# Performance work log

Hardware: AMD Instinct MI355X
Metric: run time of the kernel (lower is better)

## Reference

```python
import jax, jax.numpy as jnp
import numpy as np

N_NODES = 100000


def gcn_conv(x, W, b, src, dst, n_nodes):
    # PyG GCNConv: x' = D^{-1/2} (A + I) D^{-1/2} (x W) + b, deg counts self-loops
    h = x @ W  # [N, out]
    deg = jax.ops.segment_sum(jnp.ones_like(dst, dtype=h.dtype), dst, num_segments=n_nodes) + 1.0
    dinv = jax.lax.rsqrt(deg)  # [N]
    norm = dinv[src] * dinv[dst]  # per-edge norm [E]
    msg = h[src] * norm[:, None]  # gather + scale, [E, out]
    agg = jax.ops.segment_sum(msg, dst, num_segments=n_nodes)
    agg = agg + h * (dinv * dinv)[:, None]  # self-loop contribution
    return agg + b


def setup_inputs() -> dict:
    key = jax.random.key(0)
    ks = jax.random.split(key, 9)
    N, E, D = N_NODES, 3200000, 165
    x = jax.random.normal(ks[0], (N, D), dtype=jnp.float32)
    edge_index = jax.random.randint(ks[1], (2, E), 0, N, dtype=jnp.int64)
    def glorot(k, fan_in, fan_out):
        lim = np.sqrt(6.0 / (fan_in + fan_out))
        return jax.random.uniform(k, (fan_in, fan_out), jnp.float32, -lim, lim)
    return {
        "x": x,
        "edge_index": edge_index,
        "W1": glorot(ks[2], D, 32), "b1": jnp.zeros((32,), jnp.float32),
        "W2": glorot(ks[3], 32, 16), "b2": jnp.zeros((16,), jnp.float32),
        "W3": glorot(ks[4], 16, 2),  "b3": jnp.zeros((2,), jnp.float32),
    }


def reference(x, edge_index, W1, b1, W2, b2, W3, b3):
    src, dst = edge_index[0], edge_index[1]
    n = x.shape[0]
    h = jax.nn.relu(gcn_conv(x, W1, b1, src, dst, n))
    # dropout p=0.3 is a no-op in eval mode (training=False)
    h = jax.nn.relu(gcn_conv(h, W2, b2, src, dst, n))
    h = gcn_conv(h, W3, b3, src, dst, n)
    return jax.nn.log_softmax(h, axis=1)
```

## Files before the change

### kernel.cpp

```cpp
#include <hip/hip_runtime.h>
#include <math.h>


constexpr int NT = 256;
constexpr int NPB = 256;
constexpr int LOG_NPB = 8;
constexpr int MAXBUK = 512;
constexpr int BSTRIDE = 10240;
constexpr int NREP = 8;
constexpr int SUB = BSTRIDE / NREP;
constexpr int EPB_B = 4096;

typedef __attribute__((ext_vector_type(8))) short bf16x8;
typedef __attribute__((ext_vector_type(4))) float f32x4;

__device__ inline unsigned short f2bf(float f) {
    unsigned u = *(unsigned*)&f;
    u += 0x7fffu + ((u >> 16) & 1u);
    return (unsigned short)(u >> 16);
}
__device__ inline unsigned packbf(float a, float b) {
    return (unsigned)f2bf(a) | ((unsigned)f2bf(b) << 16);
}
__device__ inline void acc8(float* a, uint4 v) {
    const unsigned* u = (const unsigned*)&v;
#pragma unroll
    for (int w = 0; w < 4; w++) {
        unsigned lo = u[w] << 16, hi = u[w] & 0xffff0000u;
        a[2 * w]     += *(float*)&lo;
        a[2 * w + 1] += *(float*)&hi;
    }
}

__global__ __launch_bounds__(NT) void place_kernel(const int* __restrict__ src,
                                                   const int* __restrict__ dst,
                                                   int* __restrict__ cursor8,
                                                   unsigned* __restrict__ ebuf,
                                                   int E, int nbuk) {
    __shared__ int lh[MAXBUK];
    __shared__ int lbase[MAXBUK];
    for (int i = threadIdx.x; i < nbuk; i += NT) lh[i] = 0;
    __syncthreads();
    constexpr int EPT = EPB_B / NT;
    unsigned pk[EPT];
    unsigned bl[EPT];
    int base = blockIdx.x * EPB_B;
    int rep = blockIdx.x & (NREP - 1);
#pragma unroll
    for (int i = 0; i < EPT; i++) {
        int e = base + i * NT + threadIdx.x;
        if (e < E) {
            int s = src[e], d = dst[e];
            int b = d >> LOG_NPB;
            int lp = atomicAdd(&lh[b], 1);
            pk[i] = ((unsigned)(d & (NPB - 1)) << 24) | (unsigned)s;
            bl[i] = ((unsigned)b << 16) | (unsigned)lp;
        } else {
            bl[i] = 0xFFFFFFFFu;
        }
    }
    __syncthreads();
    for (int i = threadIdx.x; i < nbuk; i += NT) {
        int v = lh[i];
        if (v) lbase[i] = atomicAdd(&cursor8[rep * MAXBUK + i], v);
    }
    __syncthreads();
#pragma unroll
    for (int i = 0; i < EPT; i++) {
        if (bl[i] != 0xFFFFFFFFu) {
            int b = (int)(bl[i] >> 16);
            int pos = lbase[b] + (int)(bl[i] & 0xFFFFu);
            if (pos < SUB)
                ebuf[(size_t)b * BSTRIDE + rep * SUB + pos] = pk[i];
        }
    }
}

__global__ __launch_bounds__(NT) void sort_kernel(
    const unsigned* __restrict__ ebuf, const int* __restrict__ cursor8,
    int* __restrict__ esrc, int* __restrict__ rowptr, int* __restrict__ rowcnt,
    float* __restrict__ dinv, int N) {
    __shared__ int cnt[NPB];
    __shared__ int ofs[NPB];
    __shared__ int cur[NPB];
    int tid = threadIdx.x;
    int b = blockIdx.x;
    cnt[tid] = 0;
    __syncthreads();
#pragma unroll
    for (int r = 0; r < NREP; r++) {
        int e0 = b * BSTRIDE + r * SUB;
        int e1 = e0 + min(cursor8[r * MAXBUK + b], SUB);
        for (int i = e0 + tid; i < e1; i += NT)
            atomicAdd(&cnt[ebuf[i] >> 24], 1);
    }
    __syncthreads();
    ofs[tid] = cnt[tid];
    __syncthreads();
    for (int off = 1; off < NPB; off <<= 1) {
        int a = (tid >= off) ? ofs[tid - off] : 0;
        __syncthreads();
        ofs[tid] += a;
        __syncthreads();
    }
    {
        int excl = ofs[tid] - cnt[tid];
        cur[tid] = excl;
        int n = b * NPB + tid;
        if (n < N) {
            rowptr[n] = b * BSTRIDE + excl;
            rowcnt[n] = cnt[tid];
            dinv[n] = rsqrtf((float)cnt[tid] + 1.0f);
        }
    }
    __syncthreads();
#pragma unroll
    for (int r = 0; r < NREP; r++) {
        int e0 = b * BSTRIDE + r * SUB;
        int e1 = e0 + min(cursor8[r * MAXBUK + b], SUB);
        for (int i = e0 + tid; i < e1; i += NT) {
            unsigned p = ebuf[i];
            int l = (int)(p >> 24);
            int pos = atomicAdd(&cur[l], 1);
            esrc[b * BSTRIDE + pos] = (int)(p & 0xFFFFFFu);
        }
    }
}

__global__ __launch_bounds__(NT) void gemm1_mfma(
    const float* __restrict__ in, const float* __restrict__ W,
    const float* __restrict__ dinv, uint4* __restrict__ hs, int Ntot) {
    constexpr int DIN = 165, DOUT = 32;
    __shared__ float tile[4][16][36];
    int lane = threadIdx.x & 63;
    int wv = threadIdx.x >> 6;
    int t = blockIdx.x * 4 + wv;
    int ntiles = (Ntot + 15) >> 4;
    if (t >= ntiles) return;
    int n0 = t << 4;
    int mrow = lane & 15;
    int quad = lane >> 4;
    int arow = n0 + mrow;
    if (arow >= Ntot) arow = Ntot - 1;
    const float* xrow = in + (size_t)arow * DIN;
    f32x4 acc0 = {0.f, 0.f, 0.f, 0.f};
    f32x4 acc1 = {0.f, 0.f, 0.f, 0.f};
#pragma unroll
    for (int c = 0; c < 6; c++) {
        int kb = c * 32 + quad * 8;
        union { bf16x8 v; unsigned short u[8]; } A, B0, B1;
#pragma unroll
        for (int j = 0; j < 8; j++) {
            int k = kb + j;
            float xv = (k < DIN) ? xrow[k] : 0.f;
            float w0 = (k < DIN) ? W[k * DOUT + mrow] : 0.f;
            float w1 = (k < DIN) ? W[k * DOUT + 16 + mrow] : 0.f;
            A.u[j] = f2bf(xv);
            B0.u[j] = f2bf(w0);
            B1.u[j] = f2bf(w1);
        }
        acc0 = __builtin_amdgcn_mfma_f32_16x16x32_bf16(A.v, B0.v, acc0, 0, 0, 0);
        acc1 = __builtin_amdgcn_mfma_f32_16x16x32_bf16(A.v, B1.v, acc1, 0, 0, 0);
    }
#pragma unroll
    for (int r = 0; r < 4; r++) {
        tile[wv][quad * 4 + r][mrow] = acc0[r];
        tile[wv][quad * 4 + r][16 + mrow] = acc1[r];
    }
    int node = lane >> 2;
    int part = lane & 3;
    int n = n0 + node;
    if (n >= Ntot) return;
    float dv = dinv[n];
    float f[8];
#pragma unroll
    for (int i = 0; i < 8; i++) f[i] = tile[wv][node][part * 8 + i];
    unsigned u0 = packbf(dv * f[0], dv * f[1]);
    unsigned u1 = packbf(dv * f[2], dv * f[3]);
    unsigned u2 = packbf(dv * f[4], dv * f[5]);
    unsigned u3 = packbf(dv * f[6], dv * f[7]);
    hs[(size_t)n * 4 + part] = make_uint4(u0, u1, u2, u3);
}

__global__ __launch_bounds__(NT) void g1g2_kernel(
    const uint4* __restrict__ hsb, const int* __restrict__ esrc,
    const int* __restrict__ rowptr, const int* __restrict__ rowcnt,
    const float* __restrict__ dinv, const float* __restrict__ b1,
    const float* __restrict__ W2 , uint4* __restrict__ hs2b,
    int N) {
    __shared__ float sW[32 * 16];
    __shared__ float sb[32];
    for (int i = threadIdx.x; i < 32 * 16; i += NT) sW[i] = W2[i];
    if (threadIdx.x < 32) sb[threadIdx.x] = b1[threadIdx.x];
    __syncthreads();
    int gid = blockIdx.x * NT + threadIdx.x;
    int n = gid >> 2;
    int q = gid & 3;
    int c = q & 1;
    int h = q >> 1;
    if (n >= N) return;
    int start = rowptr[n];
    int cnt = rowcnt[n];
    int half0 = (cnt + 1) >> 1;
    int j    = start + (h ? half0 : 0);
    int jend = start + (h ? cnt : half0);
    float a[16];
    if (h == 0) {
        const uint4* hp = hsb + (size_t)n * 4 + c * 2;
        uint4 v0 = hp[0], v1 = hp[1];
        const unsigned* u0 = (const unsigned*)&v0;
        const unsigned* u1 = (const unsigned*)&v1;
#pragma unroll
        for (int w = 0; w < 4; w++) {
            unsigned lo = u0[w] << 16, hi = u0[w] & 0xffff0000u;
            a[2 * w] = *(float*)&lo; a[2 * w + 1] = *(float*)&hi;
            unsigned lo1 = u1[w] << 16, hi1 = u1[w] & 0xffff0000u;
            a[8 + 2 * w] = *(float*)&lo1; a[8 + 2 * w + 1] = *(float*)&hi1;
        }
    } else {
#pragma unroll
        for (int k = 0; k < 16; k++) a[k] = 0.f;
    }
    for (; j + 3 < jend; j += 4) {
        int s0 = esrc[j], s1 = esrc[j + 1], s2 = esrc[j + 2], s3 = esrc[j + 3];
        uint4 v00 = hsb[(size_t)s0 * 4 + c * 2], v01 = hsb[(size_t)s0 * 4 + c * 2 + 1];
        uint4 v10 = hsb[(size_t)s1 * 4 + c * 2], v11 = hsb[(size_t)s1 * 4 + c * 2 + 1];
        uint4 v20 = hsb[(size_t)s2 * 4 + c * 2], v21 = hsb[(size_t)s2 * 4 + c * 2 + 1];
        uint4 v30 = hsb[(size_t)s3 * 4 + c * 2], v31 = hsb[(size_t)s3 * 4 + c * 2 + 1];
        acc8(a, v00); acc8(a + 8, v01);
        acc8(a, v10); acc8(a + 8, v11);
        acc8(a, v20); acc8(a + 8, v21);
        acc8(a, v30); acc8(a + 8, v31);
    }
    for (; j < jend; j++) {
        int s = esrc[j];
        acc8(a, hsb[(size_t)s * 4 + c * 2]);
        acc8(a + 8, hsb[(size_t)s * 4 + c * 2 + 1]);
    }
#pragma unroll
    for (int k = 0; k < 16; k++) a[k] += __shfl_xor(a[k], 2);
    float dv = dinv[n];
    float z[16];
#pragma unroll
    for (int d = 0; d < 16; d++) z[d] = 0.f;
#pragma unroll
    for (int k = 0; k < 16; k++) {
        float f = fmaxf(fmaf(dv, a[k], sb[c * 16 + k]), 0.f);
#pragma unroll
        for (int d = 0; d < 16; d++)
            z[d] = fmaf(f, sW[(c * 16 + k) * 16 + d], z[d]);
    }
#pragma unroll
    for (int d = 0; d < 16; d++) z[d] += __shfl_xor(z[d], 1);
    if (h == 0) {
        unsigned u0 = packbf(dv * z[c * 8 + 0], dv * z[c * 8 + 1]);
        unsigned u1 = packbf(dv * z[c * 8 + 2], dv * z[c * 8 + 3]);
        unsigned u2 = packbf(dv * z[c * 8 + 4], dv * z[c * 8 + 5]);
        unsigned u3 = packbf(dv * z[c * 8 + 6], dv * z[c * 8 + 7]);
        hs2b[(size_t)n * 2 + c] = make_uint4(u0, u1, u2, u3);
    }
}

__global__ __launch_bounds__(NT) void g2g3_kernel(
    const uint4* __restrict__ hs2b, const int* __restrict__ esrc,
    const int* __restrict__ rowptr, const int* __restrict__ rowcnt,
    const float* __restrict__ dinv, const float* __restrict__ b2,
    const float* __restrict__ W3 , float* __restrict__ hs3,
    int N) {
    __shared__ float sW[32];
    __shared__ float sb[16];
    if (threadIdx.x < 32) sW[threadIdx.x] = W3[threadIdx.x];
    if (threadIdx.x < 16) sb[threadIdx.x] = b2[threadIdx.x];
    __syncthreads();
    int gid = blockIdx.x * NT + threadIdx.x;
    int n = gid >> 2;
    int q = gid & 3;
    int c = q & 1;
    int h = q >> 1;
    if (n >= N) return;
    int start = rowptr[n];
    int cnt = rowcnt[n];
    int half0 = (cnt + 1) >> 1;
    int j    = start + (h ? half0 : 0);
    int jend = start + (h ? cnt : half0);
    float a[8];
    if (h == 0) {
        uint4 v = hs2b[(size_t)n * 2 + c];
        const unsigned* u = (const unsigned*)&v;
#pragma unroll
        for (int w = 0; w < 4; w++) {
            unsigned lo = u[w] << 16, hi = u[w] & 0xffff0000u;
            a[2 * w] = *(float*)&lo; a[2 * w + 1] = *(float*)&hi;
        }
    } else {
#pragma unroll
        for (int k = 0; k < 8; k++) a[k] = 0.f;
    }
    for (; j + 3 < jend; j += 4) {
        uint4 v0 = hs2b[(size_t)esrc[j] * 2 + c];
        uint4 v1 = hs2b[(size_t)esrc[j + 1] * 2 + c];
        uint4 v2 = hs2b[(size_t)esrc[j + 2] * 2 + c];
        uint4 v3 = hs2b[(size_t)esrc[j + 3] * 2 + c];
        acc8(a, v0); acc8(a, v1); acc8(a, v2); acc8(a, v3);
    }
    for (; j < jend; j++) acc8(a, hs2b[(size_t)esrc[j] * 2 + c]);
#pragma unroll
    for (int k = 0; k < 8; k++) a[k] += __shfl_xor(a[k], 2);
    float dv = dinv[n];
    float z0 = 0.f, z1 = 0.f;
#pragma unroll
    for (int k = 0; k < 8; k++) {
        float f = fmaxf(fmaf(dv, a[k], sb[c * 8 + k]), 0.f);
        z0 = fmaf(f, sW[(c * 8 + k) * 2 + 0], z0);
        z1 = fmaf(f, sW[(c * 8 + k) * 2 + 1], z1);
    }
    z0 += __shfl_xor(z0, 1);
    z1 += __shfl_xor(z1, 1);
    if (q == 0) {
        hs3[(size_t)n * 2 + 0] = dv * z0;
        hs3[(size_t)n * 2 + 1] = dv * z1;
    }
}

__global__ __launch_bounds__(NT) void final_kernel(
    const float* __restrict__ hs3, const int* __restrict__ esrc,
    const int* __restrict__ rowptr, const int* __restrict__ rowcnt,
    const float* __restrict__ dinv, const float* __restrict__ b,
    float* __restrict__ out, int N) {
    int gid = blockIdx.x * NT + threadIdx.x;
    int n = gid >> 1;
    int h = gid & 1;
    if (n >= N) return;
    int start = rowptr[n];
    int cnt = rowcnt[n];
    int half0 = (cnt + 1) >> 1;
    int j    = start + (h ? half0 : 0);
    int jend = start + (h ? cnt : half0);
    const float2* h2 = (const float2*)hs3;
    float2 acc = h ? make_float2(0.f, 0.f) : h2[n];
    for (; j + 3 < jend; j += 4) {
        float2 v0 = h2[esrc[j]], v1 = h2[esrc[j + 1]];
        float2 v2 = h2[esrc[j + 2]], v3 = h2[esrc[j + 3]];
        acc.x += v0.x + v1.x + v2.x + v3.x;
        acc.y += v0.y + v1.y + v2.y + v3.y;
    }
    for (; j < jend; j++) {
        float2 v = h2[esrc[j]];
        acc.x += v.x; acc.y += v.y;
    }
    acc.x += __shfl_xor(acc.x, 1);
    acc.y += __shfl_xor(acc.y, 1);
    if (h == 0) {
        float dv = dinv[n];
        float z0 = fmaf(dv, acc.x, b[0]);
        float z1 = fmaf(dv, acc.y, b[1]);
        float m = fmaxf(z0, z1);
        float lse = m + logf(expf(z0 - m) + expf(z1 - m));
        out[(size_t)n * 2 + 0] = z0 - lse;
        out[(size_t)n * 2 + 1] = z1 - lse;
    }
}

extern "C" void kernel_launch(void* const* d_in, const int* in_sizes, int n_in,
                              void* d_out, int out_size, void* d_ws, size_t ws_size,
                              hipStream_t stream) {
    const float* x  = (const float*)d_in[0];
    const int*   ei = (const int*)d_in[1];
    const float* W1 = (const float*)d_in[2];
    const float* b1 = (const float*)d_in[3];
    const float* W2 = (const float*)d_in[4];
    const float* b2 = (const float*)d_in[5];
    const float* W3 = (const float*)d_in[6];
    const float* b3 = (const float*)d_in[7];
    float* out = (float*)d_out;

    const int N = in_sizes[0] / 165;
    const int E = in_sizes[1] / 2;
    const int* src = ei;
    const int* dst = ei + E;
    const int nbuk = (N + NPB - 1) >> LOG_NPB;
    const int G4 = ((size_t)N * 4 + NT - 1) / NT;
    const int G2 = ((size_t)N * 2 + NT - 1) / NT;

    char* p = (char*)d_ws;
    int* cursor8   = (int*)p;      p += (size_t)NREP * MAXBUK * 4;
    unsigned* ebuf = (unsigned*)p; p += (size_t)nbuk * BSTRIDE * 4;
    int* esrc      = (int*)p;      p += (size_t)nbuk * BSTRIDE * 4;
    int* rowptr    = (int*)p;      p += (size_t)N * 4;
    int* rowcnt    = (int*)p;      p += (size_t)N * 4;
    float* dinv    = (float*)p;    p += (size_t)N * 4;
    uint4* hs1b    = (uint4*)p;    p += (size_t)N * 4 * 16;
    uint4* hs2b    = (uint4*)p;    p += (size_t)N * 2 * 16;
    float* hs3     = (float*)p;    p += (size_t)N * 2 * 4;

    (void)hipMemsetAsync(cursor8, 0, (size_t)NREP * MAXBUK * sizeof(int), stream);
    place_kernel<<<(E + EPB_B - 1) / EPB_B, NT, 0, stream>>>(src, dst, cursor8, ebuf, E, nbuk);
    sort_kernel<<<nbuk, NT, 0, stream>>>(ebuf, cursor8, esrc, rowptr, rowcnt, dinv, N);

    gemm1_mfma<<<((N + 15) / 16 + 3) / 4, NT, 0, stream>>>(x, W1, dinv, hs1b, N);

    g1g2_kernel<<<G4, NT, 0, stream>>>(hs1b, esrc, rowptr, rowcnt, dinv, b1, W2, hs2b, N);

    g2g3_kernel<<<G4, NT, 0, stream>>>(hs2b, esrc, rowptr, rowcnt, dinv, b2, W3, hs3, N);

    final_kernel<<<G2, NT, 0, stream>>>(hs3, esrc, rowptr, rowcnt, dinv, b3, out, N);
}
```

Measured before the change: 279.6 us.

## Split layer-1 features into two channel halves with separate aggregation blocks

The layer-1 bf16 features are stored as two separate 16-channel arrays (hsA/hsB). Alternating blocks of the aggregation kernel each gather only one half, so each gathered working set is smaller and more cache-resident. Partial products with W2 go to fp32 scratch buffers, and a new combine kernel sums them, scales them and packs them to bf16. Index loads are also switched to nontemporal loads. This adds an extra kernel launch and extra scratch traffic, and each edge list is now read twice by different blocks.

```diff
diff --git a/kernel.cpp b/kernel.cpp
--- a/kernel.cpp
+++ b/kernel.cpp
@@ -50,7 +50,8 @@
     for (int i = 0; i < EPT; i++) {
         int e = base + i * NT + threadIdx.x;
         if (e < E) {
-            int s = src[e], d = dst[e];
+            int s = __builtin_nontemporal_load(src + e);
+            int d = __builtin_nontemporal_load(dst + e);
             int b = d >> LOG_NPB;
             int lp = atomicAdd(&lh[b], 1);
             pk[i] = ((unsigned)(d & (NPB - 1)) << 24) | (unsigned)s;
@@ -129,7 +130,8 @@
 
 __global__ __launch_bounds__(NT) void gemm1_mfma(
     const float* __restrict__ in, const float* __restrict__ W,
-    const float* __restrict__ dinv, uint4* __restrict__ hs, int Ntot) {
+    const float* __restrict__ dinv, uint4* __restrict__ hsA,
+    uint4* __restrict__ hsB, int Ntot) {
     constexpr int DIN = 165, DOUT = 32;
     __shared__ float tile[4][16][36];
     int lane = threadIdx.x & 63;
@@ -179,25 +181,27 @@
     unsigned u1 = packbf(dv * f[2], dv * f[3]);
     unsigned u2 = packbf(dv * f[4], dv * f[5]);
     unsigned u3 = packbf(dv * f[6], dv * f[7]);
-    hs[(size_t)n * 4 + part] = make_uint4(u0, u1, u2, u3);
+    uint4* dst = (part >> 1) ? hsB : hsA;
+    dst[(size_t)n * 2 + (part & 1)] = make_uint4(u0, u1, u2, u3);
 }
 
 __global__ __launch_bounds__(NT) void g1g2_kernel(
-    const uint4* __restrict__ hsb, const int* __restrict__ esrc,
-    const int* __restrict__ rowptr, const int* __restrict__ rowcnt,
-    const float* __restrict__ dinv, const float* __restrict__ b1,
-    const float* __restrict__ W2 , uint4* __restrict__ hs2b,
-    int N) {
+    const uint4* __restrict__ hsA, const uint4* __restrict__ hsB,
+    const int* __restrict__ esrc, const int* __restrict__ rowptr,
+    const int* __restrict__ rowcnt, const float* __restrict__ dinv,
+    const float* __restrict__ b1, const float* __restrict__ W2 ,
+    float* __restrict__ z0, float* __restrict__ z1, int N) {
     __shared__ float sW[32 * 16];
     __shared__ float sb[32];
     for (int i = threadIdx.x; i < 32 * 16; i += NT) sW[i] = W2[i];
     if (threadIdx.x < 32) sb[threadIdx.x] = b1[threadIdx.x];
     __syncthreads();
-    int gid = blockIdx.x * NT + threadIdx.x;
-    int n = gid >> 2;
-    int q = gid & 3;
-    int c = q & 1;
-    int h = q >> 1;
+    int c = blockIdx.x & 1;
+    const uint4* hsc = c ? hsB : hsA;
+    float* zc = c ? z1 : z0;
+    int t = threadIdx.x;
+    int n = (blockIdx.x >> 1) * (NT / 2) + (t >> 1);
+    int h = t & 1;
     if (n >= N) return;
     int start = rowptr[n];
     int cnt = rowcnt[n];
@@ -205,60 +209,66 @@
     int j    = start + (h ? half0 : 0);
     int jend = start + (h ? cnt : half0);
     float a[16];
-    if (h == 0) {
-        const uint4* hp = hsb + (size_t)n * 4 + c * 2;
-        uint4 v0 = hp[0], v1 = hp[1];
-        const unsigned* u0 = (const unsigned*)&v0;
-        const unsigned* u1 = (const unsigned*)&v1;
-#pragma unroll
-        for (int w = 0; w < 4; w++) {
-            unsigned lo = u0[w] << 16, hi = u0[w] & 0xffff0000u;
-            a[2 * w] = *(float*)&lo; a[2 * w + 1] = *(float*)&hi;
-            unsigned lo1 = u1[w] << 16, hi1 = u1[w] & 0xffff0000u;
-            a[8 + 2 * w] = *(float*)&lo1; a[8 + 2 * w + 1] = *(float*)&hi1;
-        }
-    } else {
-#pragma unroll
-        for (int k = 0; k < 16; k++) a[k] = 0.f;
+#pragma unroll
+    for (int k = 0; k < 16; k++) a[k] = 0.f;
+    {
+        uint4 v = hsc[(size_t)n * 2 + h];
+        acc8(a + h * 8, v);
     }
     for (; j + 3 < jend; j += 4) {
-        int s0 = esrc[j], s1 = esrc[j + 1], s2 = esrc[j + 2], s3 = esrc[j + 3];
-        uint4 v00 = hsb[(size_t)s0 * 4 + c * 2], v01 = hsb[(size_t)s0 * 4 + c * 2 + 1];
-        uint4 v10 = hsb[(size_t)s1 * 4 + c * 2], v11 = hsb[(size_t)s1 * 4 + c * 2 + 1];
-        uint4 v20 = hsb[(size_t)s2 * 4 + c * 2], v21 = hsb[(size_t)s2 * 4 + c * 2 + 1];
-        uint4 v30 = hsb[(size_t)s3 * 4 + c * 2], v31 = hsb[(size_t)s3 * 4 + c * 2 + 1];
+        int s0 = __builtin_nontemporal_load(esrc + j);
+        int s1 = __builtin_nontemporal_load(esrc + j + 1);
+        int s2 = __builtin_nontemporal_load(esrc + j + 2);
+        int s3 = __builtin_nontemporal_load(esrc + j + 3);
+        uint4 v00 = hsc[(size_t)s0 * 2], v01 = hsc[(size_t)s0 * 2 + 1];
+        uint4 v10 = hsc[(size_t)s1 * 2], v11 = hsc[(size_t)s1 * 2 + 1];
+        uint4 v20 = hsc[(size_t)s2 * 2], v21 = hsc[(size_t)s2 * 2 + 1];
+        uint4 v30 = hsc[(size_t)s3 * 2], v31 = hsc[(size_t)s3 * 2 + 1];
         acc8(a, v00); acc8(a + 8, v01);
         acc8(a, v10); acc8(a + 8, v11);
         acc8(a, v20); acc8(a + 8, v21);
         acc8(a, v30); acc8(a + 8, v31);
     }
     for (; j < jend; j++) {
-        int s = esrc[j];
-        acc8(a, hsb[(size_t)s * 4 + c * 2]);
-        acc8(a + 8, hsb[(size_t)s * 4 + c * 2 + 1]);
-    }
-#pragma unroll
-    for (int k = 0; k < 16; k++) a[k] += __shfl_xor(a[k], 2);
+        int s = __builtin_nontemporal_load(esrc + j);
+        acc8(a, hsc[(size_t)s * 2]);
+        acc8(a + 8, hsc[(size_t)s * 2 + 1]);
+    }
+#pragma unroll
+    for (int k = 0; k < 16; k++) a[k] += __shfl_xor(a[k], 1);
     float dv = dinv[n];
-    float z[16];
-#pragma unroll
-    for (int d = 0; d < 16; d++) z[d] = 0.f;
+    float z[8];
+#pragma unroll
+    for (int d = 0; d < 8; d++) z[d] = 0.f;
 #pragma unroll
     for (int k = 0; k < 16; k++) {
         float f = fmaxf(fmaf(dv, a[k], sb[c * 16 + k]), 0.f);
 #pragma unroll
-        for (int d = 0; d < 16; d++)
-            z[d] = fmaf(f, sW[(c * 16 + k) * 16 + d], z[d]);
-    }
-#pragma unroll
-    for (int d = 0; d < 16; d++) z[d] += __shfl_xor(z[d], 1);
-    if (h == 0) {
-        unsigned u0 = packbf(dv * z[c * 8 + 0], dv * z[c * 8 + 1]);
-        unsigned u1 = packbf(dv * z[c * 8 + 2], dv * z[c * 8 + 3]);
-        unsigned u2 = packbf(dv * z[c * 8 + 4], dv * z[c * 8 + 5]);
-        unsigned u3 = packbf(dv * z[c * 8 + 6], dv * z[c * 8 + 7]);
-        hs2b[(size_t)n * 2 + c] = make_uint4(u0, u1, u2, u3);
-    }
+        for (int d = 0; d < 8; d++)
+            z[d] = fmaf(f, sW[(c * 16 + k) * 16 + h * 8 + d], z[d]);
+    }
+    float4* zp = (float4*)(zc + (size_t)n * 16 + h * 8);
+    zp[0] = make_float4(z[0], z[1], z[2], z[3]);
+    zp[1] = make_float4(z[4], z[5], z[6], z[7]);
+}
+
+__global__ __launch_bounds__(NT) void combine_kernel(
+    const float* __restrict__ z0, const float* __restrict__ z1,
+    const float* __restrict__ dinv, uint4* __restrict__ hs2b, int N) {
+    int gid = blockIdx.x * NT + threadIdx.x;
+    int n = gid >> 1;
+    int p = gid & 1;
+    if (n >= N) return;
+    const float4* a4 = (const float4*)(z0 + (size_t)n * 16 + p * 8);
+    const float4* b4 = (const float4*)(z1 + (size_t)n * 16 + p * 8);
+    float4 a0 = a4[0], a1 = a4[1];
+    float4 b0 = b4[0], b1v = b4[1];
+    float dv = dinv[n];
+    unsigned u0 = packbf(dv * (a0.x + b0.x), dv * (a0.y + b0.y));
+    unsigned u1 = packbf(dv * (a0.z + b0.z), dv * (a0.w + b0.w));
+    unsigned u2 = packbf(dv * (a1.x + b1v.x), dv * (a1.y + b1v.y));
+    unsigned u3 = packbf(dv * (a1.z + b1v.z), dv * (a1.w + b1v.w));
+    hs2b[(size_t)n * 2 + p] = make_uint4(u0, u1, u2, u3);
 }
 
 __global__ __launch_bounds__(NT) void g2g3_kernel(
@@ -297,13 +307,20 @@
         for (int k = 0; k < 8; k++) a[k] = 0.f;
     }
     for (; j + 3 < jend; j += 4) {
-        uint4 v0 = hs2b[(size_t)esrc[j] * 2 + c];
-        uint4 v1 = hs2b[(size_t)esrc[j + 1] * 2 + c];
-        uint4 v2 = hs2b[(size_t)esrc[j + 2] * 2 + c];
-        uint4 v3 = hs2b[(size_t)esrc[j + 3] * 2 + c];
+        int s0 = __builtin_nontemporal_load(esrc + j);
+        int s1 = __builtin_nontemporal_load(esrc + j + 1);
+        int s2 = __builtin_nontemporal_load(esrc + j + 2);
+        int s3 = __builtin_nontemporal_load(esrc + j + 3);
+        uint4 v0 = hs2b[(size_t)s0 * 2 + c];
+        uint4 v1 = hs2b[(size_t)s1 * 2 + c];
+        uint4 v2 = hs2b[(size_t)s2 * 2 + c];
+        uint4 v3 = hs2b[(size_t)s3 * 2 + c];
         acc8(a, v0); acc8(a, v1); acc8(a, v2); acc8(a, v3);
     }
-    for (; j < jend; j++) acc8(a, hs2b[(size_t)esrc[j] * 2 + c]);
+    for (; j < jend; j++) {
+        int s = __builtin_nontemporal_load(esrc + j);
+        acc8(a, hs2b[(size_t)s * 2 + c]);
+    }
 #pragma unroll
     for (int k = 0; k < 8; k++) a[k] += __shfl_xor(a[k], 2);
     float dv = dinv[n];
@@ -339,13 +356,18 @@
     const float2* h2 = (const float2*)hs3;
     float2 acc = h ? make_float2(0.f, 0.f) : h2[n];
     for (; j + 3 < jend; j += 4) {
-        float2 v0 = h2[esrc[j]], v1 = h2[esrc[j + 1]];
-        float2 v2 = h2[esrc[j + 2]], v3 = h2[esrc[j + 3]];
+        int s0 = __builtin_nontemporal_load(esrc + j);
+        int s1 = __builtin_nontemporal_load(esrc + j + 1);
+        int s2 = __builtin_nontemporal_load(esrc + j + 2);
+        int s3 = __builtin_nontemporal_load(esrc + j + 3);
+        float2 v0 = h2[s0], v1 = h2[s1];
+        float2 v2 = h2[s2], v3 = h2[s3];
         acc.x += v0.x + v1.x + v2.x + v3.x;
         acc.y += v0.y + v1.y + v2.y + v3.y;
     }
     for (; j < jend; j++) {
-        float2 v = h2[esrc[j]];
+        int s = __builtin_nontemporal_load(esrc + j);
+        float2 v = h2[s];
         acc.x += v.x; acc.y += v.y;
     }
     acc.x += __shfl_xor(acc.x, 1);
@@ -381,6 +403,7 @@
     const int nbuk = (N + NPB - 1) >> LOG_NPB;
     const int G4 = ((size_t)N * 4 + NT - 1) / NT;
     const int G2 = ((size_t)N * 2 + NT - 1) / NT;
+    const int GS = 2 * ((N + (NT / 2) - 1) / (NT / 2));
 
     char* p = (char*)d_ws;
     int* cursor8   = (int*)p;      p += (size_t)NREP * MAXBUK * 4;
@@ -389,7 +412,10 @@
     int* rowptr    = (int*)p;      p += (size_t)N * 4;
     int* rowcnt    = (int*)p;      p += (size_t)N * 4;
     float* dinv    = (float*)p;    p += (size_t)N * 4;
-    uint4* hs1b    = (uint4*)p;    p += (size_t)N * 4 * 16;
+    uint4* hsA     = (uint4*)p;    p += (size_t)N * 2 * 16;
+    uint4* hsB     = (uint4*)p;    p += (size_t)N * 2 * 16;
+    float* z0      = (float*)p;    p += (size_t)N * 16 * 4;
+    float* z1      = (float*)p;    p += (size_t)N * 16 * 4;
     uint4* hs2b    = (uint4*)p;    p += (size_t)N * 2 * 16;
     float* hs3     = (float*)p;    p += (size_t)N * 2 * 4;
 
@@ -397,9 +423,10 @@
     place_kernel<<<(E + EPB_B - 1) / EPB_B, NT, 0, stream>>>(src, dst, cursor8, ebuf, E, nbuk);
     sort_kernel<<<nbuk, NT, 0, stream>>>(ebuf, cursor8, esrc, rowptr, rowcnt, dinv, N);
 
-    gemm1_mfma<<<((N + 15) / 16 + 3) / 4, NT, 0, stream>>>(x, W1, dinv, hs1b, N);
-
-    g1g2_kernel<<<G4, NT, 0, stream>>>(hs1b, esrc, rowptr, rowcnt, dinv, b1, W2, hs2b, N);
+    gemm1_mfma<<<((N + 15) / 16 + 3) / 4, NT, 0, stream>>>(x, W1, dinv, hsA, hsB, N);
+
+    g1g2_kernel<<<GS, NT, 0, stream>>>(hsA, hsB, esrc, rowptr, rowcnt, dinv, b1, W2, z0, z1, N);
+    combine_kernel<<<G2, NT, 0, stream>>>(z0, z1, dinv, hs2b, N);
 
     g2g3_kernel<<<G4, NT, 0, stream>>>(hs2b, esrc, rowptr, rowcnt, dinv, b2, W3, hs3, N);
 
```

Result: slower. 322.4 us (+15.3%).

## Stage bucket edges in LDS and sub-sort each row by source range

Applied to the files above, without the earlier changes.

The sort kernel now copies each bucket's packed edges into shared memory once, so the second pass reads LDS instead of re-reading global memory. It also counts edges per (destination, source-range) bin, with 8 source ranges per row, so each row's edge list comes out roughly grouped by source index. The grouping is meant to improve locality of the later gathers of h[src] in the aggregation kernels. In exchange it uses about 40KB more LDS per block, which can lower occupancy, and adds per-thread prefix work over the 8 bins.

```diff
diff --git a/kernel.cpp b/kernel.cpp
--- a/kernel.cpp
+++ b/kernel.cpp
@@ -10,6 +10,8 @@
 constexpr int NREP = 8;
 constexpr int SUB = BSTRIDE / NREP;
 constexpr int EPB_B = 4096;
+constexpr int R = 8;
+constexpr int RSH = 14;
 
 typedef __attribute__((ext_vector_type(8))) short bf16x8;
 typedef __attribute__((ext_vector_type(4))) float f32x4;
@@ -80,50 +82,61 @@
     const unsigned* __restrict__ ebuf, const int* __restrict__ cursor8,
     int* __restrict__ esrc, int* __restrict__ rowptr, int* __restrict__ rowcnt,
     float* __restrict__ dinv, int N) {
-    __shared__ int cnt[NPB];
-    __shared__ int ofs[NPB];
-    __shared__ int cur[NPB];
+    __shared__ unsigned se[BSTRIDE];
+    __shared__ int cnt[NPB * R];
+    __shared__ int cur[NPB * R];
+    __shared__ int psum[NT];
     int tid = threadIdx.x;
     int b = blockIdx.x;
-    cnt[tid] = 0;
-    __syncthreads();
+    for (int i = tid; i < NPB * R; i += NT) cnt[i] = 0;
+    __syncthreads();
+    int scnt[NREP], sofs[NREP];
+    int total = 0;
+#pragma unroll
+    for (int r = 0; r < NREP; r++) {
+        int v = min(cursor8[r * MAXBUK + b], SUB);
+        scnt[r] = v; sofs[r] = total; total += v;
+    }
 #pragma unroll
     for (int r = 0; r < NREP; r++) {
         int e0 = b * BSTRIDE + r * SUB;
-        int e1 = e0 + min(cursor8[r * MAXBUK + b], SUB);
-        for (int i = e0 + tid; i < e1; i += NT)
-            atomicAdd(&cnt[ebuf[i] >> 24], 1);
-    }
-    __syncthreads();
-    ofs[tid] = cnt[tid];
+        for (int i = tid; i < scnt[r]; i += NT) {
+            unsigned p = ebuf[e0 + i];
+            se[sofs[r] + i] = p;
+            atomicAdd(&cnt[(p >> 24) * R + ((p & 0xFFFFFFu) >> RSH)], 1);
+        }
+    }
+    __syncthreads();
+    int loc[R];
+    int s = 0;
+#pragma unroll
+    for (int i = 0; i < R; i++) { loc[i] = s; s += cnt[tid * R + i]; }
+    psum[tid] = s;
     __syncthreads();
     for (int off = 1; off < NPB; off <<= 1) {
-        int a = (tid >= off) ? ofs[tid - off] : 0;
+        int a = (tid >= off) ? psum[tid - off] : 0;
         __syncthreads();
-        ofs[tid] += a;
+        psum[tid] += a;
         __syncthreads();
     }
+    int excl = psum[tid] - s;
+#pragma unroll
+    for (int i = 0; i < R; i++) cur[tid * R + i] = excl + loc[i];
     {
-        int excl = ofs[tid] - cnt[tid];
-        cur[tid] = excl;
         int n = b * NPB + tid;
         if (n < N) {
             rowptr[n] = b * BSTRIDE + excl;
-            rowcnt[n] = cnt[tid];
-            dinv[n] = rsqrtf((float)cnt[tid] + 1.0f);
-        }
-    }
-    __syncthreads();
-#pragma unroll
-    for (int r = 0; r < NREP; r++) {
-        int e0 = b * BSTRIDE + r * SUB;
-        int e1 = e0 + min(cursor8[r * MAXBUK + b], SUB);
-        for (int i = e0 + tid; i < e1; i += NT) {
-            unsigned p = ebuf[i];
-            int l = (int)(p >> 24);
-            int pos = atomicAdd(&cur[l], 1);
-            esrc[b * BSTRIDE + pos] = (int)(p & 0xFFFFFFu);
-        }
+            rowcnt[n] = s;
+            dinv[n] = rsqrtf((float)s + 1.0f);
+        }
+    }
+    __syncthreads();
+    for (int i = tid; i < total; i += NT) {
+        unsigned p = se[i];
+        unsigned sidx = p & 0xFFFFFFu;
+        int bin = (int)(p >> 24) * R + (int)(sidx >> RSH);
+        int pos = atomicAdd(&cur[bin], 1);
+        esrc[b * BSTRIDE + pos] = (int)sidx;
     }
 }
 
```

New measurement: 275.7 us. Within noise of the previous version (-1.4%).
